# Performance work log

Measured on AMD Instinct MI355X. Metric: run time of the kernel, lower is better.

Reference implementation:

```python
import jax, jax.numpy as jnp
import numpy as np

NEG = -1e9

def _lstm_dir(x, w_ih, w_hh, b_ih, b_hh):
    # x: (N, T, in) -> (N, T, H); torch gate order i, f, g, o
    xi = x @ w_ih.T + (b_ih + b_hh)  # (N, T, 4H) input projection precomputed
    H = w_hh.shape[1]
    h0 = jnp.zeros((x.shape[0], H), x.dtype)
    def step(carry, xt):
        h, c = carry
        g = xt + h @ w_hh.T
        i, f, gg, o = jnp.split(g, 4, axis=-1)
        c = jax.nn.sigmoid(f) * c + jax.nn.sigmoid(i) * jnp.tanh(gg)
        h = jax.nn.sigmoid(o) * jnp.tanh(c)
        return (h, c), h
    _, ys = jax.lax.scan(step, (h0, h0), jnp.swapaxes(xi, 0, 1))
    return jnp.swapaxes(ys, 0, 1)

def _bilstm_layer(x, wif, whf, bif, bhf, wib, whb, bib, bhb):
    fwd = _lstm_dir(x, wif, whf, bif, bhf)
    bwd = _lstm_dir(x[:, ::-1], wib, whb, bib, bhb)[:, ::-1]
    return jnp.concatenate([fwd, bwd], axis=-1)

def _na1d(x, qkv_w, qkv_b, rpb, proj_w, proj_b, heads, kernel):
    # NATTEN-style 1D neighborhood attention with edge-clamped window + rel pos bias.
    N, L, Dm = x.shape
    hd = Dm // heads
    qkv = x @ qkv_w.T + qkv_b
    q, k, v = jnp.split(qkv, 3, axis=-1)
    sh = lambda t: t.reshape(N, L, heads, hd).transpose(0, 2, 1, 3)
    q, k, v = sh(q) * (hd ** -0.5), sh(k), sh(v)
    scores = jnp.einsum('nhid,nhjd->nhij', q, k)  # (N, heads, L, L)
    i = jnp.arange(L)[:, None]
    j = jnp.arange(L)[None, :]
    start = jnp.clip(i - kernel // 2, 0, L - kernel)     # window start per query
    mask = (j >= start) & (j < start + kernel)           # (L, L) neighborhood mask
    rel = jnp.clip(j - i + kernel - 1, 0, 2 * kernel - 2)
    bias = rpb[:, rel]                                   # (heads, L, L)
    scores = jnp.where(mask, scores + bias, NEG)
    attn = jax.nn.softmax(scores, axis=-1)
    out = jnp.einsum('nhij,nhjd->nhid', attn, v)
    out = out.transpose(0, 2, 1, 3).reshape(N, L, Dm)
    return out @ proj_w.T + proj_b

def setup_inputs() -> dict:
    key = jax.random.key(0)
    ks = iter(jax.random.split(key, 40))
    B, IN, T, P, Dm, H = 4, 256, 256, 88, 128, 64
    p = lambda *s: jax.random.normal(next(ks), s, jnp.float32) * 0.05
    inp = {'x': jax.random.normal(next(ks), (B, IN, T, P), jnp.float32)}
    for l, fin in (('l0', IN), ('l1', Dm)):
        for suf in ('', 'r'):
            inp['w_ih_' + l + suf] = p(4 * H, fin)
            inp['w_hh_' + l + suf] = p(4 * H, H)
            inp['b_ih_' + l + suf] = p(4 * H)
            inp['b_hh_' + l + suf] = p(4 * H)
    for tag, kz in (('t', 7), ('f', 87)):
        inp['qkv_w_' + tag] = p(3 * Dm, Dm)
        inp['qkv_b_' + tag] = p(3 * Dm)
        inp['rpb_' + tag] = p(1, 2 * kz - 1)
        inp['proj_w_' + tag] = p(Dm, Dm)
        inp['proj_b_' + tag] = p(Dm)
    return inp

def reference(x, w_ih_l0, w_hh_l0, b_ih_l0, b_hh_l0, w_ih_l0r, w_hh_l0r, b_ih_l0r, b_hh_l0r, w_ih_l1, w_hh_l1, b_ih_l1, b_hh_l1, w_ih_l1r, w_hh_l1r, b_ih_l1r, b_hh_l1r, qkv_w_t, qkv_b_t, rpb_t, proj_w_t, proj_b_t, qkv_w_f, qkv_b_f, rpb_f, proj_w_f, proj_b_f):
    B, IN, T, P = x.shape
    Dm = proj_w_t.shape[0]
    h = jnp.transpose(x, (0, 3, 2, 1)).reshape(B * P, T, IN)
    h = _bilstm_layer(h, w_ih_l0, w_hh_l0, b_ih_l0, b_hh_l0, w_ih_l0r, w_hh_l0r, b_ih_l0r, b_hh_l0r)
    h = _bilstm_layer(h, w_ih_l1, w_hh_l1, b_ih_l1, b_hh_l1, w_ih_l1r, w_hh_l1r, b_ih_l1r, b_hh_l1r)
    h = _na1d(h, qkv_w_t, qkv_b_t, rpb_t, proj_w_t, proj_b_t, 1, 7)            # time axis
    h = h.reshape(B, P, T, Dm).transpose(0, 2, 1, 3).reshape(B * T, P, Dm)
    h = _na1d(h, qkv_w_f, qkv_b_f, rpb_f, proj_w_f, proj_b_f, 1, 87)           # pitch axis
    return h.reshape(B, T, P, Dm)
```

## Files before the change

kernel.cpp:

```cpp
#include <hip/hip_runtime.h>
#include <cstdint>

#define TP 22528
#define MROWS 90112

typedef __bf16 bf16x8 __attribute__((ext_vector_type(8)));
typedef float  f32x4  __attribute__((ext_vector_type(4)));
typedef unsigned short us4v __attribute__((ext_vector_type(4)));

__device__ __forceinline__ unsigned short f2bf(float x) {
    unsigned u = __builtin_bit_cast(unsigned, x);
    return (unsigned short)((u + 0x7fffu + ((u >> 16) & 1u)) >> 16);
}
__device__ __forceinline__ float bf2f(unsigned short h) {
    return __builtin_bit_cast(float, (unsigned)h << 16);
}
__device__ __forceinline__ void cvt4(float a, float b, float c, float d,
                                     us4v& hi, us4v& lo) {
    unsigned short h0 = f2bf(a), h1 = f2bf(b), h2 = f2bf(c), h3 = f2bf(d);
    hi[0] = h0; hi[1] = h1; hi[2] = h2; hi[3] = h3;
    lo[0] = f2bf(a - bf2f(h0)); lo[1] = f2bf(b - bf2f(h1));
    lo[2] = f2bf(c - bf2f(h2)); lo[3] = f2bf(d - bf2f(h3));
}
__device__ __forceinline__ int swz(int r, int c) {
    return r * 64 + (c ^ ((r & 7) << 3));
}

template<int XVIEW>
__launch_bounds__(256, 2)
__global__ void gemm_mfma(const float* __restrict__ A, int lda,
                          const float* __restrict__ W0, const float* __restrict__ W1,
                          const float* __restrict__ b0a, const float* __restrict__ b0b,
                          const float* __restrict__ b1a, const float* __restrict__ b1b,
                          float* __restrict__ C, int ldc, int K, int splitN, int NB)
{
    __shared__ unsigned short lds[32768];
    const int AH = 0, AL = 8192, BH = 16384, BL = 24576;
    const int tid  = threadIdx.x;
    const int bid  = blockIdx.x;
    const int q8   = (int)gridDim.x >> 3;
    const int w    = (bid & 7) * q8 + (bid >> 3);
    const int nb   = w % NB;
    const int mb   = w / NB;
    const int n0   = nb * 128;
    const int m0   = mb * 128;
    const float* W; const float* ba; const float* bb; int nr0;
    if (n0 < splitN) { W = W0; ba = b0a; bb = b0b; nr0 = n0; }
    else             { W = W1; ba = b1a; bb = b1b; nr0 = n0 - splitN; }
    const int lane = tid & 63;
    const int wave = tid >> 6;
    const int wm   = wave >> 1, wn = wave & 1;
    const int lr   = lane & 15, lg = lane >> 4;
    const int bq   = m0 / TP;
    const int rt0  = m0 - bq * TP;

    f32x4 acc[4][4] = {};
    for (int ks = 0; ks < K; ks += 64) {
        if (XVIEW) {
            #pragma unroll
            for (int rep = 0; rep < 8; ++rep) {
                const int u = rep * 256 + tid;
                const int m = u & 127, kq = u >> 7;
                const float* src = A + (size_t)(bq * 256 + ks + kq * 4) * TP + rt0 + m;
                us4v hi, lo;
                cvt4(src[0], src[TP], src[2 * TP], src[3 * TP], hi, lo);
                *(us4v*)&lds[AH + swz(m, kq * 4)] = hi;
                *(us4v*)&lds[AL + swz(m, kq * 4)] = lo;
            }
        } else {
            #pragma unroll
            for (int rep = 0; rep < 8; ++rep) {
                const int u = rep * 256 + tid;
                const int m = u >> 4, kc = (u & 15) * 4;
                const float4 av = *(const float4*)(A + (size_t)(m0 + m) * lda + ks + kc);
                us4v hi, lo;
                cvt4(av.x, av.y, av.z, av.w, hi, lo);
                *(us4v*)&lds[AH + swz(m, kc)] = hi;
                *(us4v*)&lds[AL + swz(m, kc)] = lo;
            }
        }
        #pragma unroll
        for (int rep = 0; rep < 8; ++rep) {
            const int u = rep * 256 + tid;
            const int n = u >> 4, kc = (u & 15) * 4;
            const float4 wv = *(const float4*)(W + (size_t)(nr0 + n) * K + ks + kc);
            us4v hi, lo;
            cvt4(wv.x, wv.y, wv.z, wv.w, hi, lo);
            *(us4v*)&lds[BH + swz(n, kc)] = hi;
            *(us4v*)&lds[BL + swz(n, kc)] = lo;
        }
        __syncthreads();
        #pragma unroll
        for (int kk = 0; kk < 64; kk += 32) {
            bf16x8 ah[4], al[4], bh[4], bl[4];
            const int c8 = kk + lg * 8;
            #pragma unroll
            for (int mf = 0; mf < 4; ++mf) {
                const int r = wm * 64 + mf * 16 + lr;
                ah[mf] = *(const bf16x8*)&lds[AH + swz(r, c8)];
                al[mf] = *(const bf16x8*)&lds[AL + swz(r, c8)];
            }
            #pragma unroll
            for (int nf = 0; nf < 4; ++nf) {
                const int r = wn * 64 + nf * 16 + lr;
                bh[nf] = *(const bf16x8*)&lds[BH + swz(r, c8)];
                bl[nf] = *(const bf16x8*)&lds[BL + swz(r, c8)];
            }
            #pragma unroll
            for (int mf = 0; mf < 4; ++mf)
                #pragma unroll
                for (int nf = 0; nf < 4; ++nf) {
                    acc[mf][nf] = __builtin_amdgcn_mfma_f32_16x16x32_bf16(ah[mf], bh[nf], acc[mf][nf], 0, 0, 0);
                    acc[mf][nf] = __builtin_amdgcn_mfma_f32_16x16x32_bf16(ah[mf], bl[nf], acc[mf][nf], 0, 0, 0);
                    acc[mf][nf] = __builtin_amdgcn_mfma_f32_16x16x32_bf16(al[mf], bh[nf], acc[mf][nf], 0, 0, 0);
                }
        }
        __syncthreads();
    }
    #pragma unroll
    for (int nf = 0; nf < 4; ++nf) {
        const int ncol = wn * 64 + nf * 16 + lr;
        const float bias = ba[nr0 + ncol] + (bb ? bb[nr0 + ncol] : 0.0f);
        #pragma unroll
        for (int mf = 0; mf < 4; ++mf) {
            const int row = m0 + wm * 64 + mf * 16 + lg * 4;
            #pragma unroll
            for (int i = 0; i < 4; ++i)
                C[(size_t)(row + i) * ldc + n0 + ncol] = acc[mf][nf][i] + bias;
        }
    }
}

__launch_bounds__(256)
__global__ void lstm_kernel(const float* __restrict__ XI,
                            const float* __restrict__ whh_f,
                            const float* __restrict__ whh_b,
                            float* __restrict__ H)
{
    const int bid = blockIdx.x;
    const int dir = bid & 1;
    const int n   = bid >> 1;
    const int b   = n / 88, p = n - 88 * (n / 88);
    const int j   = threadIdx.x;
    const float* whh = dir ? whh_b : whh_f;
    const int j0 = dir ? 256 : 0;
    const int ho = dir ? 64 : 0;
    float w[64];
    #pragma unroll
    for (int k = 0; k < 64; k += 4) {
        const float4 wv = *(const float4*)(whh + (size_t)j * 64 + k);
        w[k] = wv.x; w[k+1] = wv.y; w[k+2] = wv.z; w[k+3] = wv.w;
    }
    __shared__ float h_sh[64];
    __shared__ float acts[256];
    if (j < 64) h_sh[j] = 0.0f;
    float c = 0.0f;
    __syncthreads();
    const size_t rowbase = (size_t)(b * 256) * 88 + p;
    for (int step = 0; step < 256; ++step) {
        const int t = dir ? (255 - step) : step;
        const size_t r = rowbase + (size_t)t * 88;
        float g = XI[r * 512 + j0 + j];
        #pragma unroll
        for (int k = 0; k < 64; k += 4) {
            const float4 h4 = *(const float4*)&h_sh[k];
            g += h4.x * w[k] + h4.y * w[k+1] + h4.z * w[k+2] + h4.w * w[k+3];
        }
        float a;
        if (j >= 128 && j < 192) {
            float e = __expf(2.0f * g);
            a = 1.0f - 2.0f / (e + 1.0f);
        } else {
            a = 1.0f / (1.0f + __expf(-g));
        }
        acts[j] = a;
        __syncthreads();
        if (j < 64) {
            float ai = acts[j], af = acts[64 + j], ag = acts[128 + j], ao = acts[192 + j];
            c = af * c + ai * ag;
            float e = __expf(2.0f * c);
            float th = 1.0f - 2.0f / (e + 1.0f);
            float h = ao * th;
            h_sh[j] = h;
            H[r * 128 + ho + j] = h;
        }
        __syncthreads();
    }
}

__launch_bounds__(256)
__global__ void na_t_kernel(const float* __restrict__ QKV,
                            const float* __restrict__ rpb,
                            float* __restrict__ OUT)
{
    const int wave = threadIdx.x >> 6;
    const int lane = threadIdx.x & 63;
    const int q = blockIdx.x * 4 + wave;
    const int b = q / TP; int rem = q - b * TP;
    const int i = rem / 88; const int p = rem - 88 * (rem / 88);
    int start = i - 3; if (start < 0) start = 0; if (start > 249) start = 249;
    const float scale = 0.08838834764831845f;
    const float* qrow = QKV + (size_t)q * 384;
    const float q0 = qrow[lane] * scale;
    const float q1 = qrow[lane + 64] * scale;
    const size_t rbase = (size_t)(b * 256) * 88 + p;
    float s[7];
    #pragma unroll
    for (int jj = 0; jj < 7; ++jj) {
        const int t = start + jj;
        const float* krow = QKV + (rbase + (size_t)t * 88) * 384 + 128;
        float part = q0 * krow[lane] + q1 * krow[lane + 64];
        part += __shfl_xor(part, 1);
        part += __shfl_xor(part, 2);
        part += __shfl_xor(part, 4);
        part += __shfl_xor(part, 8);
        part += __shfl_xor(part, 16);
        part += __shfl_xor(part, 32);
        int rel = t - i + 6; if (rel < 0) rel = 0; if (rel > 12) rel = 12;
        s[jj] = part + rpb[rel];
    }
    float m = s[0];
    #pragma unroll
    for (int jj = 1; jj < 7; ++jj) m = fmaxf(m, s[jj]);
    float sum = 0.0f;
    #pragma unroll
    for (int jj = 0; jj < 7; ++jj) { s[jj] = __expf(s[jj] - m); sum += s[jj]; }
    const float inv = 1.0f / sum;
    float o0 = 0.0f, o1 = 0.0f;
    #pragma unroll
    for (int jj = 0; jj < 7; ++jj) {
        const float* vrow = QKV + (rbase + (size_t)(start + jj) * 88) * 384 + 256;
        const float pj = s[jj] * inv;
        o0 += pj * vrow[lane];
        o1 += pj * vrow[lane + 64];
    }
    OUT[(size_t)q * 128 + lane] = o0;
    OUT[(size_t)q * 128 + lane + 64] = o1;
}

#define LPAD 133
#define SPAD 89
__launch_bounds__(256)
__global__ void na_f_kernel(const float* __restrict__ QKV,
                            const float* __restrict__ rpb,
                            float* __restrict__ OUT)
{
    __shared__ float Qs[96][LPAD];
    __shared__ float Ks[96][LPAD];
    __shared__ float Ss[96][SPAD];
    const int blk = blockIdx.x;
    const int tid = threadIdx.x;
    const size_t base = (size_t)blk * 88 * 384;
    const float scale = 0.08838834764831845f;
    for (int f = tid; f < 2816; f += 256) {
        const int row = f >> 5, c4 = (f & 31) * 4;
        const float4 qv = *(const float4*)(QKV + base + (size_t)row * 384 + c4);
        Qs[row][c4+0] = qv.x * scale; Qs[row][c4+1] = qv.y * scale;
        Qs[row][c4+2] = qv.z * scale; Qs[row][c4+3] = qv.w * scale;
        const float4 kv = *(const float4*)(QKV + base + (size_t)row * 384 + 128 + c4);
        Ks[row][c4+0] = kv.x; Ks[row][c4+1] = kv.y;
        Ks[row][c4+2] = kv.z; Ks[row][c4+3] = kv.w;
    }
    __syncthreads();
    const int tx = tid & 15, ty = tid >> 4;
    {
        float acc[6][6] = {};
        for (int kk = 0; kk < 128; ++kk) {
            float a[6], bb[6];
            #pragma unroll
            for (int i = 0; i < 6; ++i) a[i] = Qs[ty*6 + i][kk];
            #pragma unroll
            for (int j = 0; j < 6; ++j) bb[j] = Ks[tx*6 + j][kk];
            #pragma unroll
            for (int i = 0; i < 6; ++i)
                #pragma unroll
                for (int j = 0; j < 6; ++j)
                    acc[i][j] += a[i] * bb[j];
        }
        #pragma unroll
        for (int i = 0; i < 6; ++i) {
            const int qq = ty*6 + i;
            if (qq < 88) {
                #pragma unroll
                for (int j = 0; j < 6; ++j) {
                    const int k = tx*6 + j;
                    if (k < 88) Ss[qq][k] = acc[i][j];
                }
            }
        }
    }
    __syncthreads();
    for (int f = tid; f < 2816; f += 256) {
        const int row = f >> 5, c4 = (f & 31) * 4;
        const float4 vv = *(const float4*)(QKV + base + (size_t)row * 384 + 256 + c4);
        Ks[row][c4+0] = vv.x; Ks[row][c4+1] = vv.y;
        Ks[row][c4+2] = vv.z; Ks[row][c4+3] = vv.w;
    }
    if (tid < 88) {
        const int i = tid;
        const int jex = (i <= 43) ? 87 : 0;
        float m = -1e30f;
        for (int k = 0; k < 88; ++k) {
            if (k == jex) continue;
            int rel = k - i + 86; if (rel < 0) rel = 0; if (rel > 172) rel = 172;
            const float v = Ss[i][k] + rpb[rel];
            Ss[i][k] = v;
            m = fmaxf(m, v);
        }
        float sum = 0.0f;
        for (int k = 0; k < 88; ++k) {
            if (k == jex) continue;
            const float e = __expf(Ss[i][k] - m);
            Ss[i][k] = e;
            sum += e;
        }
        const float inv = 1.0f / sum;
        for (int k = 0; k < 88; ++k) Ss[i][k] = (k == jex) ? 0.0f : Ss[i][k] * inv;
    }
    __syncthreads();
    {
        float o[6][8] = {};
        for (int k = 0; k < 88; ++k) {
            float pv[6], vv[8];
            #pragma unroll
            for (int i = 0; i < 6; ++i) pv[i] = Ss[ty*6 + i][k];
            #pragma unroll
            for (int j = 0; j < 8; ++j) vv[j] = Ks[k][tx + 16*j];
            #pragma unroll
            for (int i = 0; i < 6; ++i)
                #pragma unroll
                for (int j = 0; j < 8; ++j)
                    o[i][j] += pv[i] * vv[j];
        }
        #pragma unroll
        for (int i = 0; i < 6; ++i) {
            const int qq = ty*6 + i;
            if (qq < 88) {
                float* dst = OUT + ((size_t)blk * 88 + qq) * 128;
                #pragma unroll
                for (int j = 0; j < 8; ++j) dst[tx + 16*j] = o[i][j];
            }
        }
    }
}

extern "C" void kernel_launch(void* const* d_in, const int* in_sizes, int n_in,
                              void* d_out, int out_size, void* d_ws, size_t ws_size,
                              hipStream_t stream)
{
    const float* x         = (const float*)d_in[0];
    const float* w_ih_l0   = (const float*)d_in[1];
    const float* w_hh_l0   = (const float*)d_in[2];
    const float* b_ih_l0   = (const float*)d_in[3];
    const float* b_hh_l0   = (const float*)d_in[4];
    const float* w_ih_l0r  = (const float*)d_in[5];
    const float* w_hh_l0r  = (const float*)d_in[6];
    const float* b_ih_l0r  = (const float*)d_in[7];
    const float* b_hh_l0r  = (const float*)d_in[8];
    const float* w_ih_l1   = (const float*)d_in[9];
    const float* w_hh_l1   = (const float*)d_in[10];
    const float* b_ih_l1   = (const float*)d_in[11];
    const float* b_hh_l1   = (const float*)d_in[12];
    const float* w_ih_l1r  = (const float*)d_in[13];
    const float* w_hh_l1r  = (const float*)d_in[14];
    const float* b_ih_l1r  = (const float*)d_in[15];
    const float* b_hh_l1r  = (const float*)d_in[16];
    const float* qkv_w_t   = (const float*)d_in[17];
    const float* qkv_b_t   = (const float*)d_in[18];
    const float* rpb_t     = (const float*)d_in[19];
    const float* proj_w_t  = (const float*)d_in[20];
    const float* proj_b_t  = (const float*)d_in[21];
    const float* qkv_w_f   = (const float*)d_in[22];
    const float* qkv_b_f   = (const float*)d_in[23];
    const float* rpb_f     = (const float*)d_in[24];
    const float* proj_w_f  = (const float*)d_in[25];
    const float* proj_b_f  = (const float*)d_in[26];

    float* ws  = (float*)d_ws;
    float* XI  = ws;
    float* H0  = ws + 46137344;
    float* H1  = ws + 57671680;
    float* QKV = XI;
    float* ATT = XI + (size_t)MROWS * 384;
    float* G   = H0;

    const int BIG = 1 << 30;
    const dim3 blk(256);

    gemm_mfma<1><<<dim3(2816), blk, 0, stream>>>(x, 0, w_ih_l0, w_ih_l0r,
        b_ih_l0, b_hh_l0, b_ih_l0r, b_hh_l0r, XI, 512, 256, 256, 4);
    lstm_kernel<<<dim3(704), blk, 0, stream>>>(XI, w_hh_l0, w_hh_l0r, H0);
    gemm_mfma<0><<<dim3(2816), blk, 0, stream>>>(H0, 128, w_ih_l1, w_ih_l1r,
        b_ih_l1, b_hh_l1, b_ih_l1r, b_hh_l1r, XI, 512, 128, 256, 4);
    lstm_kernel<<<dim3(704), blk, 0, stream>>>(XI, w_hh_l1, w_hh_l1r, H1);
    gemm_mfma<0><<<dim3(2112), blk, 0, stream>>>(H1, 128, qkv_w_t, qkv_w_t,
        qkv_b_t, nullptr, qkv_b_t, nullptr, QKV, 384, 128, BIG, 3);
    na_t_kernel<<<dim3(22528), blk, 0, stream>>>(QKV, rpb_t, ATT);
    gemm_mfma<0><<<dim3(704), blk, 0, stream>>>(ATT, 128, proj_w_t, proj_w_t,
        proj_b_t, nullptr, proj_b_t, nullptr, G, 128, 128, BIG, 1);
    gemm_mfma<0><<<dim3(2112), blk, 0, stream>>>(G, 128, qkv_w_f, qkv_w_f,
        qkv_b_f, nullptr, qkv_b_f, nullptr, QKV, 384, 128, BIG, 3);
    na_f_kernel<<<dim3(1024), blk, 0, stream>>>(QKV, rpb_f, ATT);
    gemm_mfma<0><<<dim3(704), blk, 0, stream>>>(ATT, 128, proj_w_f, proj_w_f,
        proj_b_f, nullptr, proj_b_f, nullptr, (float*)d_out, 128, 128, BIG, 1);
}
```

Baseline: 1.317 ms.

## Pre-split operands into bf16 hi/lo and stream GEMM tiles via global_load_lds

Producers (LSTM, attention kernels, proj GEMM) now write activations directly as bf16 hi/lo pairs. Weights are converted once by a new kernel, and x is transposed and split by a dedicated kernel. The GEMM drops in-loop fp32→bf16 conversion and instead double-buffers 32-wide K tiles with direct global-to-LDS loads and manual waitcnt/barriers. The LSTM also prefetches the next timestep's input projection and splits the recurrent dot product into four accumulators. This removes conversion ALU work and strided x reads from the GEMM hot loop, at the cost of extra launches, an extra pass over x, and more intermediate memory traffic.

```diff
diff --git a/kernel.cpp b/kernel.cpp
--- a/kernel.cpp
+++ b/kernel.cpp
@@ -6,7 +6,7 @@
 
 typedef __bf16 bf16x8 __attribute__((ext_vector_type(8)));
 typedef float  f32x4  __attribute__((ext_vector_type(4)));
-typedef unsigned short us4v __attribute__((ext_vector_type(4)));
+typedef unsigned short ushort8 __attribute__((ext_vector_type(8)));
 
 __device__ __forceinline__ unsigned short f2bf(float x) {
     unsigned u = __builtin_bit_cast(unsigned, x);
@@ -15,107 +15,157 @@
 __device__ __forceinline__ float bf2f(unsigned short h) {
     return __builtin_bit_cast(float, (unsigned)h << 16);
 }
-__device__ __forceinline__ void cvt4(float a, float b, float c, float d,
-                                     us4v& hi, us4v& lo) {
-    unsigned short h0 = f2bf(a), h1 = f2bf(b), h2 = f2bf(c), h3 = f2bf(d);
-    hi[0] = h0; hi[1] = h1; hi[2] = h2; hi[3] = h3;
-    lo[0] = f2bf(a - bf2f(h0)); lo[1] = f2bf(b - bf2f(h1));
-    lo[2] = f2bf(c - bf2f(h2)); lo[3] = f2bf(d - bf2f(h3));
-}
-__device__ __forceinline__ int swz(int r, int c) {
-    return r * 64 + (c ^ ((r & 7) << 3));
-}
-
-template<int XVIEW>
+__device__ __forceinline__ void gl16(const void* g, void* l) {
+    __builtin_amdgcn_global_load_lds(
+        (const __attribute__((address_space(1))) void*)g,
+        (__attribute__((address_space(3))) void*)l, 16, 0, 0);
+}
+
+__global__ void convert_w(const float* __restrict__ s0, const float* __restrict__ s1,
+                          const float* __restrict__ s2, const float* __restrict__ s3,
+                          const float* __restrict__ s4, const float* __restrict__ s5,
+                          const float* __restrict__ s6, const float* __restrict__ s7,
+                          unsigned short* __restrict__ WH, unsigned short* __restrict__ WL)
+{
+    const int stride = gridDim.x * blockDim.x;
+    for (int i = blockIdx.x * blockDim.x + threadIdx.x; i < 327680; i += stride) {
+        const float* s; int base;
+        if      (i <  65536) { s = s0; base = 0; }
+        else if (i < 131072) { s = s1; base = 65536; }
+        else if (i < 163840) { s = s2; base = 131072; }
+        else if (i < 196608) { s = s3; base = 163840; }
+        else if (i < 245760) { s = s4; base = 196608; }
+        else if (i < 262144) { s = s5; base = 245760; }
+        else if (i < 311296) { s = s6; base = 262144; }
+        else                 { s = s7; base = 311296; }
+        const float v = s[i - base];
+        const unsigned short h = f2bf(v);
+        WH[i] = h; WL[i] = f2bf(v - bf2f(h));
+    }
+}
+
+__launch_bounds__(256)
+__global__ void transpose_x(const float* __restrict__ x,
+                            unsigned short* __restrict__ Xh,
+                            unsigned short* __restrict__ Xl)
+{
+    __shared__ float tile[64][65];
+    const int tid = threadIdx.x;
+    const int tp0 = blockIdx.x * 64, k0 = blockIdx.y * 64, b = blockIdx.z;
+    #pragma unroll
+    for (int i = 0; i < 16; ++i) {
+        const int idx = i * 256 + tid;
+        const int kl = idx >> 6, tpl = idx & 63;
+        tile[kl][tpl] = x[(size_t)(b * 256 + k0 + kl) * TP + tp0 + tpl];
+    }
+    __syncthreads();
+    #pragma unroll
+    for (int i = 0; i < 2; ++i) {
+        const int u = i * 2048 + tid * 8;
+        const int ml = u >> 6, kl0 = u & 63;
+        ushort8 hi, lo;
+        #pragma unroll
+        for (int j = 0; j < 8; ++j) {
+            const float v = tile[kl0 + j][ml];
+            const unsigned short h = f2bf(v);
+            hi[j] = h; lo[j] = f2bf(v - bf2f(h));
+        }
+        const size_t row = (size_t)b * TP + tp0 + ml;
+        *(ushort8*)&Xh[row * 256 + k0 + kl0] = hi;
+        *(ushort8*)&Xl[row * 256 + k0 + kl0] = lo;
+    }
+}
+
+template<int OUTBF>
 __launch_bounds__(256, 2)
-__global__ void gemm_mfma(const float* __restrict__ A, int lda,
-                          const float* __restrict__ W0, const float* __restrict__ W1,
+__global__ void gemm_bf16(const unsigned short* __restrict__ Ahi,
+                          const unsigned short* __restrict__ Alo,
+                          const unsigned short* __restrict__ Whi0,
+                          const unsigned short* __restrict__ Wlo0,
+                          const unsigned short* __restrict__ Whi1,
+                          const unsigned short* __restrict__ Wlo1,
                           const float* __restrict__ b0a, const float* __restrict__ b0b,
                           const float* __restrict__ b1a, const float* __restrict__ b1b,
-                          float* __restrict__ C, int ldc, int K, int splitN, int NB)
+                          float* __restrict__ C,
+                          unsigned short* __restrict__ Chi, unsigned short* __restrict__ Clo,
+                          int ldc, int K, int splitN, int NB)
 {
     __shared__ unsigned short lds[32768];
-    const int AH = 0, AL = 8192, BH = 16384, BL = 24576;
     const int tid  = threadIdx.x;
     const int bid  = blockIdx.x;
     const int q8   = (int)gridDim.x >> 3;
-    const int w    = (bid & 7) * q8 + (bid >> 3);
-    const int nb   = w % NB;
-    const int mb   = w / NB;
+    const int wq   = (bid & 7) * q8 + (bid >> 3);
+    const int nb   = wq % NB;
+    const int mb   = wq / NB;
     const int n0   = nb * 128;
     const int m0   = mb * 128;
-    const float* W; const float* ba; const float* bb; int nr0;
-    if (n0 < splitN) { W = W0; ba = b0a; bb = b0b; nr0 = n0; }
-    else             { W = W1; ba = b1a; bb = b1b; nr0 = n0 - splitN; }
+    const unsigned short* Wh; const unsigned short* Wl;
+    const float* ba; const float* bb; int nr0;
+    if (n0 < splitN) { Wh = Whi0; Wl = Wlo0; ba = b0a; bb = b0b; nr0 = n0; }
+    else             { Wh = Whi1; Wl = Wlo1; ba = b1a; bb = b1b; nr0 = n0 - splitN; }
     const int lane = tid & 63;
-    const int wave = tid >> 6;
-    const int wm   = wave >> 1, wn = wave & 1;
+    const int wv   = tid >> 6;
+    const int wm   = wv >> 1, wn = wv & 1;
     const int lr   = lane & 15, lg = lane >> 4;
-    const int bq   = m0 / TP;
-    const int rt0  = m0 - bq * TP;
-
+    const int voff = (lane >> 2) * K + (((lane & 3) ^ ((lane >> 2) & 3)) * 8);
+    const int wb   = wv * 1024;
+
+    const unsigned short* gAh = Ahi + (size_t)(m0 + wv * 32) * K + voff;
+    const unsigned short* gAl = Alo + (size_t)(m0 + wv * 32) * K + voff;
+    const unsigned short* gBh = Wh + (size_t)(nr0 + wv * 32) * K + voff;
+    const unsigned short* gBl = Wl + (size_t)(nr0 + wv * 32) * K + voff;
+
+    const int NT = K >> 5;
     f32x4 acc[4][4] = {};
-    for (int ks = 0; ks < K; ks += 64) {
-        if (XVIEW) {
-            #pragma unroll
-            for (int rep = 0; rep < 8; ++rep) {
-                const int u = rep * 256 + tid;
-                const int m = u & 127, kq = u >> 7;
-                const float* src = A + (size_t)(bq * 256 + ks + kq * 4) * TP + rt0 + m;
-                us4v hi, lo;
-                cvt4(src[0], src[TP], src[2 * TP], src[3 * TP], hi, lo);
-                *(us4v*)&lds[AH + swz(m, kq * 4)] = hi;
-                *(us4v*)&lds[AL + swz(m, kq * 4)] = lo;
+
+    auto stage = [&](int bufi, int ks) {
+        unsigned short* base = lds + bufi * 16384;
+        gl16(gAh + ks,          base +         wb);
+        gl16(gAh + ks + 16 * K, base +         wb + 512);
+        gl16(gAl + ks,          base + 4096  + wb);
+        gl16(gAl + ks + 16 * K, base + 4096  + wb + 512);
+        gl16(gBh + ks,          base + 8192  + wb);
+        gl16(gBh + ks + 16 * K, base + 8192  + wb + 512);
+        gl16(gBl + ks,          base + 12288 + wb);
+        gl16(gBl + ks + 16 * K, base + 12288 + wb + 512);
+    };
+
+    stage(0, 0);
+    for (int t = 0; t < NT; ++t) {
+        const int cur = (t & 1) * 16384;
+        if (t + 1 < NT) {
+            stage((t & 1) ^ 1, (t + 1) * 32);
+            asm volatile("s_waitcnt vmcnt(8)" ::: "memory");
+        } else {
+            asm volatile("s_waitcnt vmcnt(0)" ::: "memory");
+        }
+        __builtin_amdgcn_s_barrier();
+        __builtin_amdgcn_sched_barrier(0);
+        bf16x8 ah[4], al[4], bh[4], bl[4];
+        #pragma unroll
+        for (int mf = 0; mf < 4; ++mf) {
+            const int r = wm * 64 + mf * 16 + lr;
+            const int o = r * 32 + ((lg ^ (r & 3)) * 8);
+            ah[mf] = *(const bf16x8*)&lds[cur + o];
+            al[mf] = *(const bf16x8*)&lds[cur + 4096 + o];
+        }
+        #pragma unroll
+        for (int nf = 0; nf < 4; ++nf) {
+            const int r = wn * 64 + nf * 16 + lr;
+            const int o = r * 32 + ((lg ^ (r & 3)) * 8);
+            bh[nf] = *(const bf16x8*)&lds[cur + 8192 + o];
+            bl[nf] = *(const bf16x8*)&lds[cur + 12288 + o];
+        }
+        #pragma unroll
+        for (int mf = 0; mf < 4; ++mf)
+            #pragma unroll
+            for (int nf = 0; nf < 4; ++nf) {
+                acc[mf][nf] = __builtin_amdgcn_mfma_f32_16x16x32_bf16(ah[mf], bh[nf], acc[mf][nf], 0, 0, 0);
+                acc[mf][nf] = __builtin_amdgcn_mfma_f32_16x16x32_bf16(ah[mf], bl[nf], acc[mf][nf], 0, 0, 0);
+                acc[mf][nf] = __builtin_amdgcn_mfma_f32_16x16x32_bf16(al[mf], bh[nf], acc[mf][nf], 0, 0, 0);
             }
-        } else {
-            #pragma unroll
-            for (int rep = 0; rep < 8; ++rep) {
-                const int u = rep * 256 + tid;
-                const int m = u >> 4, kc = (u & 15) * 4;
-                const float4 av = *(const float4*)(A + (size_t)(m0 + m) * lda + ks + kc);
-                us4v hi, lo;
-                cvt4(av.x, av.y, av.z, av.w, hi, lo);
-                *(us4v*)&lds[AH + swz(m, kc)] = hi;
-                *(us4v*)&lds[AL + swz(m, kc)] = lo;
-            }
-        }
-        #pragma unroll
-        for (int rep = 0; rep < 8; ++rep) {
-            const int u = rep * 256 + tid;
-            const int n = u >> 4, kc = (u & 15) * 4;
-            const float4 wv = *(const float4*)(W + (size_t)(nr0 + n) * K + ks + kc);
-            us4v hi, lo;
-            cvt4(wv.x, wv.y, wv.z, wv.w, hi, lo);
-            *(us4v*)&lds[BH + swz(n, kc)] = hi;
-            *(us4v*)&lds[BL + swz(n, kc)] = lo;
-        }
-        __syncthreads();
-        #pragma unroll
-        for (int kk = 0; kk < 64; kk += 32) {
-            bf16x8 ah[4], al[4], bh[4], bl[4];
-            const int c8 = kk + lg * 8;
-            #pragma unroll
-            for (int mf = 0; mf < 4; ++mf) {
-                const int r = wm * 64 + mf * 16 + lr;
-                ah[mf] = *(const bf16x8*)&lds[AH + swz(r, c8)];
-                al[mf] = *(const bf16x8*)&lds[AL + swz(r, c8)];
-            }
-            #pragma unroll
-            for (int nf = 0; nf < 4; ++nf) {
-                const int r = wn * 64 + nf * 16 + lr;
-                bh[nf] = *(const bf16x8*)&lds[BH + swz(r, c8)];
-                bl[nf] = *(const bf16x8*)&lds[BL + swz(r, c8)];
-            }
-            #pragma unroll
-            for (int mf = 0; mf < 4; ++mf)
-                #pragma unroll
-                for (int nf = 0; nf < 4; ++nf) {
-                    acc[mf][nf] = __builtin_amdgcn_mfma_f32_16x16x32_bf16(ah[mf], bh[nf], acc[mf][nf], 0, 0, 0);
-                    acc[mf][nf] = __builtin_amdgcn_mfma_f32_16x16x32_bf16(ah[mf], bl[nf], acc[mf][nf], 0, 0, 0);
-                    acc[mf][nf] = __builtin_amdgcn_mfma_f32_16x16x32_bf16(al[mf], bh[nf], acc[mf][nf], 0, 0, 0);
-                }
-        }
-        __syncthreads();
+        __builtin_amdgcn_s_barrier();
+        __builtin_amdgcn_sched_barrier(0);
     }
     #pragma unroll
     for (int nf = 0; nf < 4; ++nf) {
@@ -125,8 +175,16 @@
         for (int mf = 0; mf < 4; ++mf) {
             const int row = m0 + wm * 64 + mf * 16 + lg * 4;
             #pragma unroll
-            for (int i = 0; i < 4; ++i)
-                C[(size_t)(row + i) * ldc + n0 + ncol] = acc[mf][nf][i] + bias;
+            for (int i = 0; i < 4; ++i) {
+                const float v = acc[mf][nf][i] + bias;
+                if (OUTBF) {
+                    const size_t o = (size_t)(row + i) * ldc + n0 + ncol;
+                    const unsigned short h = f2bf(v);
+                    Chi[o] = h; Clo[o] = f2bf(v - bf2f(h));
+                } else {
+                    C[(size_t)(row + i) * ldc + n0 + ncol] = v;
+                }
+            }
         }
     }
 }
@@ -135,7 +193,8 @@
 __global__ void lstm_kernel(const float* __restrict__ XI,
                             const float* __restrict__ whh_f,
                             const float* __restrict__ whh_b,
-                            float* __restrict__ H)
+                            unsigned short* __restrict__ Hh,
+                            unsigned short* __restrict__ Hl)
 {
     const int bid = blockIdx.x;
     const int dir = bid & 1;
@@ -157,18 +216,30 @@
     float c = 0.0f;
     __syncthreads();
     const size_t rowbase = (size_t)(b * 256) * 88 + p;
+    float pref = XI[(rowbase + (size_t)(dir ? 255 : 0) * 88) * 512 + j0 + j];
     for (int step = 0; step < 256; ++step) {
         const int t = dir ? (255 - step) : step;
         const size_t r = rowbase + (size_t)t * 88;
-        float g = XI[r * 512 + j0 + j];
-        #pragma unroll
-        for (int k = 0; k < 64; k += 4) {
-            const float4 h4 = *(const float4*)&h_sh[k];
-            g += h4.x * w[k] + h4.y * w[k+1] + h4.z * w[k+2] + h4.w * w[k+3];
-        }
+        float gs0 = pref, gs1 = 0.0f, gs2 = 0.0f, gs3 = 0.0f;
+        if (step + 1 < 256) {
+            const int tn = dir ? (254 - step) : (step + 1);
+            pref = XI[(rowbase + (size_t)tn * 88) * 512 + j0 + j];
+        }
+        #pragma unroll
+        for (int k = 0; k < 64; k += 16) {
+            const float4 h0 = *(const float4*)&h_sh[k];
+            const float4 h1 = *(const float4*)&h_sh[k + 4];
+            const float4 h2 = *(const float4*)&h_sh[k + 8];
+            const float4 h3 = *(const float4*)&h_sh[k + 12];
+            gs0 += h0.x * w[k]    + h0.y * w[k+1]  + h0.z * w[k+2]  + h0.w * w[k+3];
+            gs1 += h1.x * w[k+4]  + h1.y * w[k+5]  + h1.z * w[k+6]  + h1.w * w[k+7];
+            gs2 += h2.x * w[k+8]  + h2.y * w[k+9]  + h2.z * w[k+10] + h2.w * w[k+11];
+            gs3 += h3.x * w[k+12] + h3.y * w[k+13] + h3.z * w[k+14] + h3.w * w[k+15];
+        }
+        const float g = (gs0 + gs1) + (gs2 + gs3);
         float a;
         if (j >= 128 && j < 192) {
-            float e = __expf(2.0f * g);
+            const float e = __expf(2.0f * g);
             a = 1.0f - 2.0f / (e + 1.0f);
         } else {
             a = 1.0f / (1.0f + __expf(-g));
@@ -176,13 +247,15 @@
         acts[j] = a;
         __syncthreads();
         if (j < 64) {
-            float ai = acts[j], af = acts[64 + j], ag = acts[128 + j], ao = acts[192 + j];
+            const float ai = acts[j], af = acts[64 + j], ag = acts[128 + j], ao = acts[192 + j];
             c = af * c + ai * ag;
-            float e = __expf(2.0f * c);
-            float th = 1.0f - 2.0f / (e + 1.0f);
-            float h = ao * th;
+            const float e = __expf(2.0f * c);
+            const float th = 1.0f - 2.0f / (e + 1.0f);
+            const float h = ao * th;
             h_sh[j] = h;
-            H[r * 128 + ho + j] = h;
+            const size_t o = r * 128 + ho + j;
+            const unsigned short hh = f2bf(h);
+            Hh[o] = hh; Hl[o] = f2bf(h - bf2f(hh));
         }
         __syncthreads();
     }
@@ -191,7 +264,8 @@
 __launch_bounds__(256)
 __global__ void na_t_kernel(const float* __restrict__ QKV,
                             const float* __restrict__ rpb,
-                            float* __restrict__ OUT)
+                            unsigned short* __restrict__ OUTh,
+                            unsigned short* __restrict__ OUTl)
 {
     const int wave = threadIdx.x >> 6;
     const int lane = threadIdx.x & 63;
@@ -234,8 +308,11 @@
         o0 += pj * vrow[lane];
         o1 += pj * vrow[lane + 64];
     }
-    OUT[(size_t)q * 128 + lane] = o0;
-    OUT[(size_t)q * 128 + lane + 64] = o1;
+    const size_t oi = (size_t)q * 128 + lane;
+    const unsigned short h0 = f2bf(o0);
+    OUTh[oi] = h0; OUTl[oi] = f2bf(o0 - bf2f(h0));
+    const unsigned short h1 = f2bf(o1);
+    OUTh[oi + 64] = h1; OUTl[oi + 64] = f2bf(o1 - bf2f(h1));
 }
 
 #define LPAD 133
@@ -243,7 +320,8 @@
 __launch_bounds__(256)
 __global__ void na_f_kernel(const float* __restrict__ QKV,
                             const float* __restrict__ rpb,
-                            float* __restrict__ OUT)
+                            unsigned short* __restrict__ OUTh,
+                            unsigned short* __restrict__ OUTl)
 {
     __shared__ float Qs[96][LPAD];
     __shared__ float Ks[96][LPAD];
@@ -336,9 +414,14 @@
         for (int i = 0; i < 6; ++i) {
             const int qq = ty*6 + i;
             if (qq < 88) {
-                float* dst = OUT + ((size_t)blk * 88 + qq) * 128;
+                const size_t ro = ((size_t)blk * 88 + qq) * 128;
                 #pragma unroll
-                for (int j = 0; j < 8; ++j) dst[tx + 16*j] = o[i][j];
+                for (int j = 0; j < 8; ++j) {
+                    const float v = o[i][j];
+                    const unsigned short hh = f2bf(v);
+                    OUTh[ro + tx + 16*j] = hh;
+                    OUTl[ro + tx + 16*j] = f2bf(v - bf2f(hh));
+                }
             }
         }
     }
@@ -376,31 +459,52 @@
     const float* proj_w_f  = (const float*)d_in[25];
     const float* proj_b_f  = (const float*)d_in[26];
 
-    float* ws  = (float*)d_ws;
-    float* XI  = ws;
-    float* H0  = ws + 46137344;
-    float* H1  = ws + 57671680;
-    float* QKV = XI;
-    float* ATT = XI + (size_t)MROWS * 384;
-    float* G   = H0;
+    float* ws = (float*)d_ws;
+    float*          XI   = ws;
+    float*          QKV  = ws;
+    unsigned short* ATTh = (unsigned short*)(ws + (size_t)MROWS * 384);
+    unsigned short* ATTl = ATTh + (size_t)MROWS * 128;
+    unsigned short* Hh   = (unsigned short*)(ws + 46137344);
+    unsigned short* Hl   = Hh + (size_t)MROWS * 128;
+    unsigned short* Gh   = (unsigned short*)(ws + 57671680);
+    unsigned short* Gl   = Gh + (size_t)MROWS * 128;
+    unsigned short* Xh   = (unsigned short*)(ws + 46137344);
+    unsigned short* Xl   = Xh + (size_t)MROWS * 256;
+    unsigned short* WH   = (unsigned short*)(ws + 69206016);
+    unsigned short* WL   = WH + 327680;
 
     const int BIG = 1 << 30;
     const dim3 blk(256);
 
-    gemm_mfma<1><<<dim3(2816), blk, 0, stream>>>(x, 0, w_ih_l0, w_ih_l0r,
-        b_ih_l0, b_hh_l0, b_ih_l0r, b_hh_l0r, XI, 512, 256, 256, 4);
-    lstm_kernel<<<dim3(704), blk, 0, stream>>>(XI, w_hh_l0, w_hh_l0r, H0);
-    gemm_mfma<0><<<dim3(2816), blk, 0, stream>>>(H0, 128, w_ih_l1, w_ih_l1r,
-        b_ih_l1, b_hh_l1, b_ih_l1r, b_hh_l1r, XI, 512, 128, 256, 4);
-    lstm_kernel<<<dim3(704), blk, 0, stream>>>(XI, w_hh_l1, w_hh_l1r, H1);
-    gemm_mfma<0><<<dim3(2112), blk, 0, stream>>>(H1, 128, qkv_w_t, qkv_w_t,
-        qkv_b_t, nullptr, qkv_b_t, nullptr, QKV, 384, 128, BIG, 3);
-    na_t_kernel<<<dim3(22528), blk, 0, stream>>>(QKV, rpb_t, ATT);
-    gemm_mfma<0><<<dim3(704), blk, 0, stream>>>(ATT, 128, proj_w_t, proj_w_t,
-        proj_b_t, nullptr, proj_b_t, nullptr, G, 128, 128, BIG, 1);
-    gemm_mfma<0><<<dim3(2112), blk, 0, stream>>>(G, 128, qkv_w_f, qkv_w_f,
-        qkv_b_f, nullptr, qkv_b_f, nullptr, QKV, 384, 128, BIG, 3);
-    na_f_kernel<<<dim3(1024), blk, 0, stream>>>(QKV, rpb_f, ATT);
-    gemm_mfma<0><<<dim3(704), blk, 0, stream>>>(ATT, 128, proj_w_f, proj_w_f,
-        proj_b_f, nullptr, proj_b_f, nullptr, (float*)d_out, 128, 128, BIG, 1);
-}
+    convert_w<<<dim3(320), blk, 0, stream>>>(w_ih_l0, w_ih_l0r, w_ih_l1, w_ih_l1r,
+        qkv_w_t, proj_w_t, qkv_w_f, proj_w_f, WH, WL);
+    transpose_x<<<dim3(352, 4, 4), blk, 0, stream>>>(x, Xh, Xl);
+    gemm_bf16<0><<<dim3(2816), blk, 0, stream>>>(Xh, Xl,
+        WH, WL, WH + 65536, WL + 65536,
+        b_ih_l0, b_hh_l0, b_ih_l0r, b_hh_l0r,
+        XI, nullptr, nullptr, 512, 256, 256, 4);
+    lstm_kernel<<<dim3(704), blk, 0, stream>>>(XI, w_hh_l0, w_hh_l0r, Hh, Hl);
+    gemm_bf16<0><<<dim3(2816), blk, 0, stream>>>(Hh, Hl,
+        WH + 131072, WL + 131072, WH + 163840, WL + 163840,
+        b_ih_l1, b_hh_l1, b_ih_l1r, b_hh_l1r,
+        XI, nullptr, nullptr, 512, 128, 256, 4);
+    lstm_kernel<<<dim3(704), blk, 0, stream>>>(XI, w_hh_l1, w_hh_l1r, Hh, Hl);
+    gemm_bf16<0><<<dim3(2112), blk, 0, stream>>>(Hh, Hl,
+        WH + 196608, WL + 196608, WH + 196608, WL + 196608,
+        qkv_b_t, nullptr, qkv_b_t, nullptr,
+        QKV, nullptr, nullptr, 384, 128, BIG, 3);
+    na_t_kernel<<<dim3(22528), blk, 0, stream>>>(QKV, rpb_t, ATTh, ATTl);
+    gemm_bf16<1><<<dim3(704), blk, 0, stream>>>(ATTh, ATTl,
+        WH + 245760, WL + 245760, WH + 245760, WL + 245760,
+        proj_b_t, nullptr, proj_b_t, nullptr,
+        nullptr, Gh, Gl, 128, 128, BIG, 1);
+    gemm_bf16<0><<<dim3(2112), blk, 0, stream>>>(Gh, Gl,
+        WH + 262144, WL + 262144, WH + 262144, WL + 262144,
+        qkv_b_f, nullptr, qkv_b_f, nullptr,
+        QKV, nullptr, nullptr, 384, 128, BIG, 3);
+    na_f_kernel<<<dim3(1024), blk, 0, stream>>>(QKV, rpb_f, ATTh, ATTl);
+    gemm_bf16<0><<<dim3(704), blk, 0, stream>>>(ATTh, ATTl,
+        WH + 311296, WL + 311296, WH + 311296, WL + 311296,
+        proj_b_f, nullptr, proj_b_f, nullptr,
+        (float*)d_out, nullptr, nullptr, 128, 128, BIG, 1);
+}
```

Result: faster. 1.104 ms (-16.2%).
